# Kernel tuning notes

Measured on AMD Instinct MI355X. Metric: run time of the kernel, lower is better.

## Reference

```python
import jax, jax.numpy as jnp
import numpy as np

N_NODES = 100000
NEG_SLOPE = 0.2  # PyG GATConv default


def _add_self_loops(edge_index, n):
    loop = jnp.arange(n, dtype=edge_index.dtype)
    src = jnp.concatenate([edge_index[0], loop])
    dst = jnp.concatenate([edge_index[1], loop])
    return src, dst


def _gat_conv(x, src, dst, W, a_src, a_dst, b, n):
    h = x @ W                                   # [N, d]
    alpha_src = h @ a_src                        # [N]
    alpha_dst = h @ a_dst                        # [N]
    e = alpha_src[src] + alpha_dst[dst]          # [E]
    e = jnp.where(e >= 0, e, NEG_SLOPE * e)      # LeakyReLU
    # segment softmax over incoming edges of each target node
    m = jax.ops.segment_max(e, dst, num_segments=n)   # every node has a self loop
    ex = jnp.exp(e - m[dst])
    denom = jax.ops.segment_sum(ex, dst, num_segments=n)
    alpha = ex / denom[dst]                      # [E]
    out = jax.ops.segment_sum(h[src] * alpha[:, None], dst, num_segments=n)
    return out + b


def setup_inputs() -> dict:
    key = jax.random.key(0)
    ks = jax.random.split(key, 10)
    num_feat, dim = 14, 16
    E = 3200000
    x = jax.random.normal(ks[0], (N_NODES, num_feat), dtype=jnp.float32)
    edge_index = jax.random.randint(ks[1], (2, E), 0, N_NODES, dtype=jnp.int64)
    s1 = 1.0 / np.sqrt(num_feat)
    s2 = 1.0 / np.sqrt(dim)
    return {
        "x": x,
        "edge_index": edge_index,
        "W1": jax.random.uniform(ks[2], (num_feat, dim), jnp.float32, -s1, s1),
        "a_src1": jax.random.uniform(ks[3], (dim,), jnp.float32, -s2, s2),
        "a_dst1": jax.random.uniform(ks[4], (dim,), jnp.float32, -s2, s2),
        "b1": jnp.zeros((dim,), jnp.float32),
        "W2": jax.random.uniform(ks[5], (dim, dim), jnp.float32, -s2, s2),
        "a_src2": jax.random.uniform(ks[6], (dim,), jnp.float32, -s2, s2),
        "a_dst2": jax.random.uniform(ks[7], (dim,), jnp.float32, -s2, s2),
        "b2": jnp.zeros((dim,), jnp.float32),
    }


def reference(x, edge_index, W1, a_src1, a_dst1, b1, W2, a_src2, a_dst2, b2):
    n = x.shape[0]
    src, dst = _add_self_loops(edge_index, n)
    h = _gat_conv(x, src, dst, W1, a_src1, a_dst1, b1, n)
    h = jax.nn.relu(h)
    # F.dropout in eval mode is identity
    out = _gat_conv(h, src, dst, W2, a_src2, a_dst2, b2, n)
    return out
```

## Files before the change

kernel.cpp:

```cpp
#include <hip/hip_runtime.h>
#include <hip/hip_fp16.h>

static constexpr float SLOPE = 0.2f;

#define NPB 256
#define NBMAX 512
#define CAP 10240
#define EPB 8192

__device__ __forceinline__ unsigned fkey(float f) {
    unsigned u = __float_as_uint(f);
    return (u & 0x80000000u) ? ~u : (u | 0x80000000u);
}
__device__ __forceinline__ float fdekey(unsigned k) {
    unsigned u = (k & 0x80000000u) ? (k & 0x7FFFFFFFu) : ~k;
    return __uint_as_float(u);
}

__device__ __forceinline__ int load_idx(const void* ei, int is64, long long pos) {
    return is64 ? (int)((const long long*)ei)[pos] : ((const int*)ei)[pos];
}

__global__ void zero_kernel(unsigned* __restrict__ gkeys, int* __restrict__ bfill) {
    int t = threadIdx.x;
    if (t < 2) gkeys[t] = 0u;
    for (int i = t; i < NBMAX; i += 256) bfill[i] = 0;
}

__global__ void __launch_bounds__(1024) bin_kernel(
        const void* __restrict__ ei, int* __restrict__ bfill,
        unsigned int* __restrict__ packed, int e, int nb) {
    __shared__ int hist[NBMAX];
    __shared__ int lbase[NBMAX];
    __shared__ int cur[NBMAX];
    __shared__ unsigned staged[EPB];
    __shared__ unsigned short sbkt[EPB];
    __shared__ int sflag;
    int t = threadIdx.x;
    if (t < 64) {
        unsigned hi = ((const unsigned*)ei)[2 * t + 1];
        unsigned long long b = __ballot(hi != 0u);
        if (t == 0) sflag = (b == 0ull) ? 1 : 0;
    }
    if (t < NBMAX) hist[t] = 0;
    __syncthreads();
    int is64 = sflag;
    long long e0 = (long long)blockIdx.x * EPB;
    int cnt = (int)min((long long)EPB, (long long)e - e0);
    int sr[8], dr[8];
    if (!is64 && t * 8 + 7 < cnt) {
        const uint4* ps = (const uint4*)((const int*)ei + e0) + t * 2;
        const uint4* pd = (const uint4*)((const int*)ei + e + e0) + t * 2;
        uint4 s0 = ps[0], s1 = ps[1], d0 = pd[0], d1 = pd[1];
        sr[0] = s0.x; sr[1] = s0.y; sr[2] = s0.z; sr[3] = s0.w;
        sr[4] = s1.x; sr[5] = s1.y; sr[6] = s1.z; sr[7] = s1.w;
        dr[0] = d0.x; dr[1] = d0.y; dr[2] = d0.z; dr[3] = d0.w;
        dr[4] = d1.x; dr[5] = d1.y; dr[6] = d1.z; dr[7] = d1.w;
    } else {
#pragma unroll
        for (int r = 0; r < 8; ++r) {
            int i = t * 8 + r;
            dr[r] = -1;
            if (i < cnt) {
                sr[r] = load_idx(ei, is64, e0 + i);
                dr[r] = load_idx(ei, is64, (long long)e + e0 + i);
            }
        }
    }
#pragma unroll
    for (int r = 0; r < 8; ++r)
        if (dr[r] >= 0) atomicAdd(&hist[dr[r] >> 8], 1);
    __syncthreads();
    int v = (t < NBMAX) ? hist[t] : 0;
    if (t < NBMAX) lbase[t] = v;
    __syncthreads();
    for (int off = 1; off < NBMAX; off <<= 1) {
        int y = (t < NBMAX && t >= off) ? lbase[t - off] : 0;
        __syncthreads();
        if (t < NBMAX) lbase[t] += y;
        __syncthreads();
    }
    if (t < NBMAX) {
        lbase[t] -= v;
        cur[t] = lbase[t];
        hist[t] = (v > 0) ? atomicAdd(&bfill[t], v) : 0;
    }
    __syncthreads();
#pragma unroll
    for (int r = 0; r < 8; ++r) {
        if (dr[r] >= 0) {
            int bk = dr[r] >> 8;
            int lp = atomicAdd(&cur[bk], 1);
            staged[lp] = ((unsigned)(dr[r] & 255) << 17) | (unsigned)sr[r];
            sbkt[lp] = (unsigned short)bk;
        }
    }
    __syncthreads();
    for (int i = t; i < cnt; i += 1024) {
        int bk = sbkt[i];
        int within = hist[bk] + (i - lbase[bk]);
        if (within < CAP)
            packed[(long long)bk * CAP + within] = staged[i];
    }
}

template <int NF>
__global__ void feat_kernel(const float* __restrict__ x, const float* __restrict__ W,
                            const float* __restrict__ avs, const float* __restrict__ avd,
                            float* __restrict__ h, __half* __restrict__ h16,
                            float* __restrict__ as, float* __restrict__ ad,
                            unsigned* __restrict__ gkey, int n) {
    __shared__ float sW[NF * 16];
    __shared__ float sa[32];
    __shared__ float red[256];
    int t = threadIdx.x;
    if (t < NF * 16) sW[t] = W[t];
    if (t < 16) sa[t] = avs[t];
    else if (t < 32) sa[t] = avd[t - 16];
    __syncthreads();
    int nid = blockIdx.x * blockDim.x + t;
    float s1 = -1e30f;
    if (nid < n) {
        float xi[NF];
#pragma unroll
        for (int f = 0; f < NF; ++f) xi[f] = x[(long long)nid * NF + f];
        float hv[16];
        s1 = 0.f;
        float s2 = 0.f;
#pragma unroll
        for (int k = 0; k < 16; ++k) {
            float acc = 0.f;
#pragma unroll
            for (int f = 0; f < NF; ++f) acc = fmaf(xi[f], sW[f * 16 + k], acc);
            hv[k] = acc;
            s1 = fmaf(acc, sa[k], s1);
            s2 = fmaf(acc, sa[16 + k], s2);
        }
        float4* hp = (float4*)(h + (long long)nid * 16);
        hp[0] = make_float4(hv[0], hv[1], hv[2], hv[3]);
        hp[1] = make_float4(hv[4], hv[5], hv[6], hv[7]);
        hp[2] = make_float4(hv[8], hv[9], hv[10], hv[11]);
        hp[3] = make_float4(hv[12], hv[13], hv[14], hv[15]);
        unsigned u[8];
#pragma unroll
        for (int q = 0; q < 8; ++q) {
            __half2 p2 = __halves2half2(__float2half(hv[2 * q]), __float2half(hv[2 * q + 1]));
            u[q] = *(unsigned*)&p2;
        }
        uint4* hp16 = (uint4*)(h16 + (long long)nid * 16);
        hp16[0] = make_uint4(u[0], u[1], u[2], u[3]);
        hp16[1] = make_uint4(u[4], u[5], u[6], u[7]);
        as[nid] = s1;
        ad[nid] = s2;
    }
    red[t] = s1;
    __syncthreads();
    for (int off = 128; off > 0; off >>= 1) {
        if (t < off) red[t] = fmaxf(red[t], red[t + off]);
        __syncthreads();
    }
    if (t == 0) atomicMax(gkey, fkey(red[0]));
}

__global__ void __launch_bounds__(1024) aggr_kernel(
        const float* __restrict__ h, const __half* __restrict__ h16,
        const float* __restrict__ as, const float* __restrict__ ad,
        const unsigned* __restrict__ packed, const int* __restrict__ bfill,
        const float* __restrict__ bias, const unsigned* __restrict__ gkey,
        float* __restrict__ out, int n, int do_relu) {
    __shared__ unsigned long long accS[NPB * 17];
    __shared__ unsigned long long denS[NPB];
    __shared__ float ccS[NPB];
    __shared__ float adnS[NPB];
    int b = blockIdx.x, t = threadIdx.x;
    float gmax = fdekey(*gkey);
    if (t < NPB) {
        int node = b * NPB + t;
        if (node < n) {
            float adn = ad[node];
            adnS[t] = adn;
            float gm = gmax + adn;
            float m = fmaxf(gm, SLOPE * gm);
            float es = as[node] + adn;
            es = fmaxf(es, SLOPE * es);
            float kb = fminf(7.f, fmaxf(0.f, floorf((m - es) * 1.44269504f)));
            float cc = (21.f + kb) * 0.69314718f - m;
            ccS[t] = cc;
            float ws = __expf(es + cc);
            denS[t] = (unsigned long long)(long long)(int)ws;
            const float4* hp = (const float4*)(h + (long long)node * 16);
            float4 h0 = hp[0], h1v = hp[1], h2v = hp[2], h3v = hp[3];
            float hv[16] = {h0.x, h0.y, h0.z, h0.w, h1v.x, h1v.y, h1v.z, h1v.w,
                            h2v.x, h2v.y, h2v.z, h2v.w, h3v.x, h3v.y, h3v.z, h3v.w};
#pragma unroll
            for (int k = 0; k < 16; ++k)
                accS[t * 17 + k] = (unsigned long long)(long long)(int)(ws * hv[k]);
        }
    }
    __syncthreads();
    int cnt = min(bfill[b], CAP);
    long long pb = (long long)b * CAP;
#pragma unroll 2
    for (int j = t; j < cnt; j += 1024) {
        unsigned p = packed[pb + j];
        int dl = p >> 17;
        int s = (int)(p & 0x1FFFF);
        float e2 = as[s] + adnS[dl];
        e2 = fmaxf(e2, SLOPE * e2);
        float w = __expf(e2 + ccS[dl]);
        atomicAdd(&denS[dl], (unsigned long long)(long long)(int)w);
        const uint4* hr = (const uint4*)(h16 + (long long)s * 16);
        uint4 r0 = hr[0], r1 = hr[1];
        unsigned rr[8] = {r0.x, r0.y, r0.z, r0.w, r1.x, r1.y, r1.z, r1.w};
        int base = dl * 17;
#pragma unroll
        for (int q = 0; q < 8; ++q) {
            __half2 h2 = *(__half2*)&rr[q];
            float2 f = __half22float2(h2);
            atomicAdd(&accS[base + 2 * q],
                      (unsigned long long)(long long)(int)(w * f.x));
            atomicAdd(&accS[base + 2 * q + 1],
                      (unsigned long long)(long long)(int)(w * f.y));
        }
    }
    __syncthreads();
    for (int idx = t; idx < NPB * 16; idx += 1024) {
        int i = idx >> 4, k = idx & 15;
        int node = b * NPB + i;
        if (node < n) {
            float o = (float)(long long)accS[i * 17 + k] /
                      (float)(long long)denS[i] + bias[k];
            if (do_relu) o = fmaxf(o, 0.f);
            out[(long long)node * 16 + k] = o;
        }
    }
}

extern "C" void kernel_launch(void* const* d_in, const int* in_sizes, int n_in,
                              void* d_out, int out_size, void* d_ws, size_t ws_size,
                              hipStream_t stream) {
    const float* x  = (const float*)d_in[0];
    const void*  ei = d_in[1];
    const float* W1  = (const float*)d_in[2];
    const float* as1 = (const float*)d_in[3];
    const float* ad1 = (const float*)d_in[4];
    const float* b1  = (const float*)d_in[5];
    const float* W2  = (const float*)d_in[6];
    const float* as2 = (const float*)d_in[7];
    const float* ad2 = (const float*)d_in[8];
    const float* b2  = (const float*)d_in[9];
    float* out = (float*)d_out;

    const int n = in_sizes[0] / 14;
    const int e = in_sizes[1] / 2;
    const int nb = (n + NPB - 1) / NPB;

    char* p = (char*)d_ws;
    auto alloc = [&](size_t bytes) {
        char* r = p;
        p += (bytes + 255) & ~(size_t)255;
        return r;
    };
    unsigned* gkeys  = (unsigned*)alloc(256);
    int*      bfill  = (int*)alloc(NBMAX * 4);
    unsigned* packed = (unsigned*)alloc((size_t)nb * CAP * 4);
    float*    h      = (float*)alloc((size_t)n * 16 * 4);
    __half*   h16    = (__half*)alloc((size_t)n * 16 * 2);
    float*    h1     = (float*)alloc((size_t)n * 16 * 4);
    float*    asb    = (float*)alloc((size_t)n * 4);
    float*    adb    = (float*)alloc((size_t)n * 4);

    zero_kernel<<<1, 256, 0, stream>>>(gkeys, bfill);
    bin_kernel<<<(e + EPB - 1) / EPB, 1024, 0, stream>>>(ei, bfill, packed, e, nb);

    feat_kernel<14><<<(n + 255) / 256, 256, 0, stream>>>(x, W1, as1, ad1, h, h16, asb, adb, gkeys + 0, n);
    aggr_kernel<<<nb, 1024, 0, stream>>>(h, h16, asb, adb, packed, bfill, b1, gkeys + 0, h1, n, 1);
    feat_kernel<16><<<(n + 255) / 256, 256, 0, stream>>>(h1, W2, as2, ad2, h, h16, asb, adb, gkeys + 1, n);
    aggr_kernel<<<nb, 1024, 0, stream>>>(h, h16, asb, adb, packed, bfill, b2, gkeys + 1, out, n, 0);
}
```

Measured before the change: 138.0 us.

## Compute exact per-node segment max and pack pairs of fixed-point accumulators per atomic

Replaces the global-max-based softmax offset with an exact per-destination max, computed in shared memory by a first pass over the bucket's edges. Edge data is kept in registers (up to 10 per thread) for the second pass. Two 32-bit fixed-point feature sums are packed into one 64-bit shared atomic with a bias trick, and the denominator and edge count share another word, halving the atomic count. This drops the global max reduction from feat_kernel but adds an extra pass, atomicMax traffic, and a carry-decoding step whose overflow handling is delicate.

```diff
diff --git a/kernel.cpp b/kernel.cpp
--- a/kernel.cpp
+++ b/kernel.cpp
@@ -112,115 +112,134 @@
                             unsigned* __restrict__ gkey, int n) {
     __shared__ float sW[NF * 16];
     __shared__ float sa[32];
-    __shared__ float red[256];
     int t = threadIdx.x;
     if (t < NF * 16) sW[t] = W[t];
     if (t < 16) sa[t] = avs[t];
     else if (t < 32) sa[t] = avd[t - 16];
     __syncthreads();
     int nid = blockIdx.x * blockDim.x + t;
-    float s1 = -1e30f;
-    if (nid < n) {
-        float xi[NF];
-#pragma unroll
-        for (int f = 0; f < NF; ++f) xi[f] = x[(long long)nid * NF + f];
-        float hv[16];
-        s1 = 0.f;
-        float s2 = 0.f;
-#pragma unroll
-        for (int k = 0; k < 16; ++k) {
-            float acc = 0.f;
-#pragma unroll
-            for (int f = 0; f < NF; ++f) acc = fmaf(xi[f], sW[f * 16 + k], acc);
-            hv[k] = acc;
-            s1 = fmaf(acc, sa[k], s1);
-            s2 = fmaf(acc, sa[16 + k], s2);
-        }
-        float4* hp = (float4*)(h + (long long)nid * 16);
-        hp[0] = make_float4(hv[0], hv[1], hv[2], hv[3]);
-        hp[1] = make_float4(hv[4], hv[5], hv[6], hv[7]);
-        hp[2] = make_float4(hv[8], hv[9], hv[10], hv[11]);
-        hp[3] = make_float4(hv[12], hv[13], hv[14], hv[15]);
-        unsigned u[8];
-#pragma unroll
-        for (int q = 0; q < 8; ++q) {
-            __half2 p2 = __halves2half2(__float2half(hv[2 * q]), __float2half(hv[2 * q + 1]));
-            u[q] = *(unsigned*)&p2;
-        }
-        uint4* hp16 = (uint4*)(h16 + (long long)nid * 16);
-        hp16[0] = make_uint4(u[0], u[1], u[2], u[3]);
-        hp16[1] = make_uint4(u[4], u[5], u[6], u[7]);
-        as[nid] = s1;
-        ad[nid] = s2;
-    }
-    red[t] = s1;
-    __syncthreads();
-    for (int off = 128; off > 0; off >>= 1) {
-        if (t < off) red[t] = fmaxf(red[t], red[t + off]);
-        __syncthreads();
-    }
-    if (t == 0) atomicMax(gkey, fkey(red[0]));
+    if (nid >= n) return;
+    float xi[NF];
+#pragma unroll
+    for (int f = 0; f < NF; ++f) xi[f] = x[(long long)nid * NF + f];
+    float hv[16];
+    float s1 = 0.f, s2 = 0.f;
+#pragma unroll
+    for (int k = 0; k < 16; ++k) {
+        float acc = 0.f;
+#pragma unroll
+        for (int f = 0; f < NF; ++f) acc = fmaf(xi[f], sW[f * 16 + k], acc);
+        hv[k] = acc;
+        s1 = fmaf(acc, sa[k], s1);
+        s2 = fmaf(acc, sa[16 + k], s2);
+    }
+    float4* hp = (float4*)(h + (long long)nid * 16);
+    hp[0] = make_float4(hv[0], hv[1], hv[2], hv[3]);
+    hp[1] = make_float4(hv[4], hv[5], hv[6], hv[7]);
+    hp[2] = make_float4(hv[8], hv[9], hv[10], hv[11]);
+    hp[3] = make_float4(hv[12], hv[13], hv[14], hv[15]);
+    unsigned u[8];
+#pragma unroll
+    for (int q = 0; q < 8; ++q) {
+        __half2 p2 = __halves2half2(__float2half(hv[2 * q]), __float2half(hv[2 * q + 1]));
+        u[q] = *(unsigned*)&p2;
+    }
+    uint4* hp16 = (uint4*)(h16 + (long long)nid * 16);
+    hp16[0] = make_uint4(u[0], u[1], u[2], u[3]);
+    hp16[1] = make_uint4(u[4], u[5], u[6], u[7]);
+    as[nid] = s1;
+    ad[nid] = s2;
 }
 
 __global__ void __launch_bounds__(1024) aggr_kernel(
         const float* __restrict__ h, const __half* __restrict__ h16,
         const float* __restrict__ as, const float* __restrict__ ad,
         const unsigned* __restrict__ packed, const int* __restrict__ bfill,
-        const float* __restrict__ bias, const unsigned* __restrict__ gkey,
+        const float* __restrict__ bias,
         float* __restrict__ out, int n, int do_relu) {
-    __shared__ unsigned long long accS[NPB * 17];
-    __shared__ unsigned long long denS[NPB];
+    __shared__ unsigned long long accS[NPB * 9];
+    __shared__ unsigned maxS[NPB];
     __shared__ float ccS[NPB];
     __shared__ float adnS[NPB];
     int b = blockIdx.x, t = threadIdx.x;
-    float gmax = fdekey(*gkey);
+    int cnt = min(bfill[b], CAP);
+    long long pb = (long long)b * CAP;
+    if (t < NPB) {
+        int node = b * NPB + t;
+        float adn = (node < n) ? ad[node] : 0.f;
+        adnS[t] = adn;
+        float es = (node < n) ? (as[node] + adn) : 0.f;
+        es = fmaxf(es, SLOPE * es);
+        maxS[t] = fkey(es);
+    }
+    __syncthreads();
+    unsigned pk[10];
+    float ev[10];
+#pragma unroll
+    for (int r = 0; r < 10; ++r) {
+        int j = t + r * 1024;
+        pk[r] = 0xFFFFFFFFu;
+        if (j < cnt) {
+            unsigned p = packed[pb + j];
+            int dl = p >> 17;
+            int s = (int)(p & 0x1FFFF);
+            float e2 = as[s] + adnS[dl];
+            e2 = fmaxf(e2, SLOPE * e2);
+            pk[r] = p;
+            ev[r] = e2;
+            atomicMax(&maxS[dl], fkey(e2));
+        }
+    }
+    __syncthreads();
     if (t < NPB) {
         int node = b * NPB + t;
         if (node < n) {
-            float adn = ad[node];
-            adnS[t] = adn;
-            float gm = gmax + adn;
-            float m = fmaxf(gm, SLOPE * gm);
-            float es = as[node] + adn;
+            float m = fdekey(maxS[t]);
+            float cc = 21.f * 0.69314718f - m;
+            ccS[t] = cc;
+            float es = as[node] + adnS[t];
             es = fmaxf(es, SLOPE * es);
-            float kb = fminf(7.f, fmaxf(0.f, floorf((m - es) * 1.44269504f)));
-            float cc = (21.f + kb) * 0.69314718f - m;
-            ccS[t] = cc;
             float ws = __expf(es + cc);
-            denS[t] = (unsigned long long)(long long)(int)ws;
+            unsigned wsi = (unsigned)(int)ws;
+            int base = t * 9;
             const float4* hp = (const float4*)(h + (long long)node * 16);
             float4 h0 = hp[0], h1v = hp[1], h2v = hp[2], h3v = hp[3];
             float hv[16] = {h0.x, h0.y, h0.z, h0.w, h1v.x, h1v.y, h1v.z, h1v.w,
                             h2v.x, h2v.y, h2v.z, h2v.w, h3v.x, h3v.y, h3v.z, h3v.w};
 #pragma unroll
-            for (int k = 0; k < 16; ++k)
-                accS[t * 17 + k] = (unsigned long long)(long long)(int)(ws * hv[k]);
-        }
-    }
-    __syncthreads();
-    int cnt = min(bfill[b], CAP);
-    long long pb = (long long)b * CAP;
-#pragma unroll 2
-    for (int j = t; j < cnt; j += 1024) {
-        unsigned p = packed[pb + j];
-        int dl = p >> 17;
-        int s = (int)(p & 0x1FFFF);
-        float e2 = as[s] + adnS[dl];
-        e2 = fmaxf(e2, SLOPE * e2);
-        float w = __expf(e2 + ccS[dl]);
-        atomicAdd(&denS[dl], (unsigned long long)(long long)(int)w);
-        const uint4* hr = (const uint4*)(h16 + (long long)s * 16);
-        uint4 r0 = hr[0], r1 = hr[1];
-        unsigned rr[8] = {r0.x, r0.y, r0.z, r0.w, r1.x, r1.y, r1.z, r1.w};
-        int base = dl * 17;
-#pragma unroll
-        for (int q = 0; q < 8; ++q) {
-            __half2 h2 = *(__half2*)&rr[q];
-            float2 f = __half22float2(h2);
-            atomicAdd(&accS[base + 2 * q],
-                      (unsigned long long)(long long)(int)(w * f.x));
-            atomicAdd(&accS[base + 2 * q + 1],
-                      (unsigned long long)(long long)(int)(w * f.y));
+            for (int q = 0; q < 8; ++q) {
+                int t0 = (int)(ws * hv[2 * q]);
+                int t1 = (int)(ws * hv[2 * q + 1]);
+                accS[base + q] = ((unsigned long long)(unsigned)t1 << 32) +
+                                 (unsigned long long)((unsigned)t0 + 0x80000000u);
+            }
+            accS[base + 8] = (1ull << 32) | wsi;
+        }
+    }
+    __syncthreads();
+#pragma unroll
+    for (int r = 0; r < 10; ++r) {
+        if (pk[r] != 0xFFFFFFFFu) {
+            unsigned p = pk[r];
+            int dl = p >> 17;
+            int s = (int)(p & 0x1FFFF);
+            float w = __expf(ev[r] + ccS[dl]);
+            unsigned wi = (unsigned)(int)w;
+            int base = dl * 9;
+            atomicAdd(&accS[base + 8], (1ull << 32) | wi);
+            const uint4* hr = (const uint4*)(h16 + (long long)s * 16);
+            uint4 r0 = hr[0], r1 = hr[1];
+            unsigned rr[8] = {r0.x, r0.y, r0.z, r0.w, r1.x, r1.y, r1.z, r1.w};
+#pragma unroll
+            for (int q = 0; q < 8; ++q) {
+                float2 f = __half22float2(*(__half2*)&rr[q]);
+                int t0 = (int)(w * f.x);
+                int t1 = (int)(w * f.y);
+                unsigned long long enc =
+                    ((unsigned long long)(unsigned)t1 << 32) +
+                    (unsigned long long)((unsigned)t0 + 0x80000000u);
+                atomicAdd(&accS[base + q], enc);
+            }
         }
     }
     __syncthreads();
@@ -228,8 +247,22 @@
         int i = idx >> 4, k = idx & 15;
         int node = b * NPB + i;
         if (node < n) {
-            float o = (float)(long long)accS[i * 17 + k] /
-                      (float)(long long)denS[i] + bias[k];
+            unsigned long long dpack = accS[i * 9 + 8];
+            unsigned kcnt = (unsigned)(dpack >> 32);
+            float den = (float)(unsigned)dpack;
+            unsigned long long a = accS[i * 9 + (k >> 1)];
+            unsigned lo = (unsigned)a, hi = (unsigned)(a >> 32);
+            int s0 = (int)(lo - (kcnt << 31));
+            float val;
+            if ((k & 1) == 0) {
+                val = (float)s0;
+            } else {
+                long long carries =
+                    ((((long long)kcnt) << 31) + (long long)s0) >> 32;
+                int s1 = (int)(hi - (unsigned)carries);
+                val = (float)s1;
+            }
+            float o = val / den + bias[k];
             if (do_relu) o = fmaxf(o, 0.f);
             out[(long long)node * 16 + k] = o;
         }
@@ -274,7 +307,7 @@
     bin_kernel<<<(e + EPB - 1) / EPB, 1024, 0, stream>>>(ei, bfill, packed, e, nb);
 
     feat_kernel<14><<<(n + 255) / 256, 256, 0, stream>>>(x, W1, as1, ad1, h, h16, asb, adb, gkeys + 0, n);
-    aggr_kernel<<<nb, 1024, 0, stream>>>(h, h16, asb, adb, packed, bfill, b1, gkeys + 0, h1, n, 1);
+    aggr_kernel<<<nb, 1024, 0, stream>>>(h, h16, asb, adb, packed, bfill, b1, h1, n, 1);
     feat_kernel<16><<<(n + 255) / 256, 256, 0, stream>>>(h1, W2, as2, ad2, h, h16, asb, adb, gkeys + 1, n);
-    aggr_kernel<<<nb, 1024, 0, stream>>>(h, h16, asb, adb, packed, bfill, b2, gkeys + 1, out, n, 0);
-}
+    aggr_kernel<<<nb, 1024, 0, stream>>>(h, h16, asb, adb, packed, bfill, b2, gkeys + 1 ? out : out, n, 0);
+}
```

Measured after the change: 120.8 us. -12.4%, faster.
